# Performance work log

Hardware: AMD Instinct MI355X
Metric: run time of the kernel (lower is better)

## Reference

```python
import jax, jax.numpy as jnp
import numpy as np
import math

N = 50000
E = 1600000
A = 100          # num_atoms
H = 64           # hidden_dim / node_dim
L = 5            # num_layers
NB = 8           # num_basis
LMAX = 2
CUTOFF = 5.0


def setup_inputs() -> dict:
    key = jax.random.key(0)
    ks = jax.random.split(key, 32)
    s = 0.05
    inp = {
        'atomic_numbers': jax.random.randint(ks[0], (N,), 0, A),
        'pos': jax.random.normal(ks[1], (N, 3), jnp.float32) * 2.0,
        'edge_index': jax.random.randint(ks[2], (2, E), 0, N),
        # GaussianBasis widths
        'widths': jnp.ones((NB,), jnp.float32) * 0.5,
        # node embedding
        'embed': jax.random.normal(ks[3], (A, H), jnp.float32),
        # per-layer params, stacked on leading layer dim
        'rad_w1': jax.random.normal(ks[4], (L, NB, H), jnp.float32) * s,
        'rad_b1': jnp.zeros((L, H), jnp.float32),
        'rad_w2': jax.random.normal(ks[5], (L, H, H * (LMAX + 1)), jnp.float32) * s,
        'rad_b2': jnp.zeros((L, H * (LMAX + 1)), jnp.float32),
        'self_w': jax.random.normal(ks[6], (L, H, H), jnp.float32) * s,
        'self_b': jnp.zeros((L, H), jnp.float32),
        'proj_w': jax.random.normal(ks[7], (L, 2 * H, H), jnp.float32) * s,
        'proj_b': jnp.zeros((L, H), jnp.float32),
        'mlp_w1': jax.random.normal(ks[8], (L, H, 2 * H), jnp.float32) * s,
        'mlp_b1': jnp.zeros((L, 2 * H), jnp.float32),
        'mlp_w2': jax.random.normal(ks[9], (L, 2 * H, H), jnp.float32) * s,
        'mlp_b2': jnp.zeros((L, H), jnp.float32),
        'ln_g': jnp.ones((L, H), jnp.float32),
        'ln_b': jnp.zeros((L, H), jnp.float32),
        # readout MLP
        'ro_w1': jax.random.normal(ks[10], (H, H), jnp.float32) * s,
        'ro_b1': jnp.zeros((H,), jnp.float32),
        'ro_w2': jax.random.normal(ks[11], (H, H // 2), jnp.float32) * s,
        'ro_b2': jnp.zeros((H // 2,), jnp.float32),
        'ro_w3': jax.random.normal(ks[12], (H // 2, 1), jnp.float32) * s,
        'ro_b3': jnp.zeros((1,), jnp.float32),
        # per-species reference energies
        'atomic_e': jax.random.normal(ks[13], (A, 1), jnp.float32) * s,
    }
    return inp


def _layer_norm(x, g, b, eps=1e-5):
    mu = jnp.mean(x, axis=-1, keepdims=True)
    var = jnp.var(x, axis=-1, keepdims=True)
    return (x - mu) * jax.lax.rsqrt(var + eps) * g + b


def _spherical_harmonics(edge_vec):
    # real SH up to lmax=2, [E, 9] (computed for fidelity; unused by conv math)
    r = jnp.clip(jnp.linalg.norm(edge_vec, axis=-1), 1e-8, None)
    x, y, z = edge_vec[:, 0] / r, edge_vec[:, 1] / r, edge_vec[:, 2] / r
    x2, y2, z2 = x * x, y * y, z * z
    return jnp.stack([
        jnp.full_like(x, 0.28209479177387814),
        -0.4886025119029199 * y, 0.4886025119029199 * z, -0.4886025119029199 * x,
        1.0925484305920792 * x * y, -1.0925484305920792 * y * z,
        0.94617469575756 * z2 - 0.31539156525252 * (x2 + y2),
        -1.0925484305920792 * x * z, 0.5462742152960396 * (x2 - y2),
    ], axis=-1)


def _forward(atomic_numbers, pos, edge_index, widths, embed,
             rad_w1, rad_b1, rad_w2, rad_b2, self_w, self_b, proj_w, proj_b,
             mlp_w1, mlp_b1, mlp_w2, mlp_b2, ln_g, ln_b,
             ro_w1, ro_b1, ro_w2, ro_b2, ro_w3, ro_b3, atomic_e):
    n = pos.shape[0]
    row, col = edge_index[0], edge_index[1]
    edge_vec = pos[col] - pos[row]                          # [E,3]
    edge_len = jnp.linalg.norm(edge_vec, axis=-1, keepdims=True)  # [E,1]

    # GaussianBasis
    xr = edge_len / CUTOFF
    cut = 0.5 * (jnp.cos(xr * math.pi) + 1.0)
    cut = cut * (edge_len < CUTOFF).astype(jnp.float32)     # [E,1]
    centers = jnp.linspace(0.0, CUTOFF, NB)
    diff = edge_len - centers                               # [E,NB]
    edge_rbf = jnp.exp(-0.5 * (diff / jnp.clip(widths, 0.1, None)) ** 2) * cut

    edge_sh = _spherical_harmonics(edge_vec)  # computed but unused, as in source

    feats = embed[atomic_numbers]                           # [N,H]
    for i in range(L):
        # radial net -> per-edge weights [E, H*(lmax+1)]
        w = jax.nn.silu(edge_rbf @ rad_w1[i] + rad_b1[i]) @ rad_w2[i] + rad_b2[i]
        # messages: node_j[:,:,None] * w.view(E,H,lmax+1) summed over last dim
        # == node_j * w.reshape(E,H,lmax+1).sum(-1)
        wsum = w.reshape(-1, H, LMAX + 1).sum(axis=-1)      # [E,H]
        messages = feats[col] * wsum                        # gather + multiply
        agg = jax.ops.segment_sum(messages, row, num_segments=n)  # scatter-add
        self_out = feats @ self_w[i] + self_b[i]
        conv_out = jnp.concatenate([self_out, agg], axis=-1) @ proj_w[i] + proj_b[i]
        upd = jax.nn.silu(conv_out @ mlp_w1[i] + mlp_b1[i]) @ mlp_w2[i] + mlp_b2[i]
        feats = _layer_norm(feats + upd, ln_g[i], ln_b[i])

    h = jax.nn.silu(feats @ ro_w1 + ro_b1)
    h = jax.nn.silu(h @ ro_w2 + ro_b2)
    atomic_energies = h @ ro_w3 + ro_b3                     # [N,1]
    atomic_energies = atomic_energies + atomic_e[atomic_numbers]
    return atomic_energies.sum()                            # batch=None path


def reference(atomic_numbers, pos, edge_index, widths, embed,
              rad_w1, rad_b1, rad_w2, rad_b2, self_w, self_b, proj_w, proj_b,
              mlp_w1, mlp_b1, mlp_w2, mlp_b2, ln_g, ln_b,
              ro_w1, ro_b1, ro_w2, ro_b2, ro_w3, ro_b3, atomic_e):
    return _forward(atomic_numbers, pos, edge_index, widths, embed,
                    rad_w1, rad_b1, rad_w2, rad_b2, self_w, self_b, proj_w, proj_b,
                    mlp_w1, mlp_b1, mlp_w2, mlp_b2, ln_g, ln_b,
                    ro_w1, ro_b1, ro_w2, ro_b2, ro_w3, ro_b3, atomic_e)
```

## Files before the change

kernel.cpp:

```cpp
#include <hip/hip_runtime.h>
#include <math.h>

constexpr int N_NODES = 50000;
constexpr int N_EDGES = 1600000;
constexpr int HDIM    = 64;
constexpr int NLAYER  = 5;
constexpr int NBASIS  = 8;
constexpr int TLUT    = 512;
constexpr float CUT_R = 5.0f;
constexpr float PI_F  = 3.14159265358979f;

constexpr int NBKT = 196;
constexpr int BCAP = 9216;
constexpr int TILE = 1024;

typedef __attribute__((ext_vector_type(8))) short short8;
typedef __attribute__((ext_vector_type(4))) float f32x4;
#define MFMA16 __builtin_amdgcn_mfma_f32_16x16x32_bf16

__device__ __forceinline__ float waveRedSum(float v) {
    for (int off = 32; off > 0; off >>= 1) v += __shfl_xor(v, off, 64);
    return v;
}
__device__ __forceinline__ float siluf(float x) { return x / (1.0f + __expf(-x)); }

__device__ __forceinline__ unsigned int f2bf(float x) {
    unsigned int b = __float_as_uint(x);
    return (b + 0x7fffu + ((b >> 16) & 1u)) >> 16;
}
__device__ __forceinline__ float bf_lo(unsigned int u) { return __uint_as_float(u << 16); }
__device__ __forceinline__ float bf_hi(unsigned int u) { return __uint_as_float(u & 0xffff0000u); }


__global__ void k_embed(const int* __restrict__ an, const float* __restrict__ embed,
                        float* __restrict__ feats, unsigned short* __restrict__ featsbf) {
    int i = blockIdx.x * blockDim.x + threadIdx.x;
    if (i >= N_NODES * HDIM) return;
    int node = i >> 6, h = i & 63;
    float v = embed[an[node] * HDIM + h];
    feats[i] = v;
    featsbf[i] = (unsigned short)f2bf(v);
}

__global__ __launch_bounds__(256) void k_binA(const int* __restrict__ row,
                                              const int* __restrict__ col,
                                              const float* __restrict__ pos,
                                              int* __restrict__ btail,
                                              uint2* __restrict__ binned) {
    __shared__ uint2 ent[TILE];
    __shared__ short bb[TILE];
    __shared__ uint2 sorted[TILE];
    __shared__ int cnt[256], cnt2[256], base[256], gbase[256], scn[256];
    const int tid = threadIdx.x;
    const int t0  = blockIdx.x * TILE;
    const int nv  = min(TILE, N_EDGES - t0);

    cnt[tid] = 0;
    __syncthreads();

    #pragma unroll
    for (int i = 0; i < TILE / 256; ++i) {
        int idx = i * 256 + tid;
        if (idx < nv) {
            int e = t0 + idx;
            int r = row[e], c = col[e];
            float dx = pos[c * 3 + 0] - pos[r * 3 + 0];
            float dy = pos[c * 3 + 1] - pos[r * 3 + 1];
            float dz = pos[c * 3 + 2] - pos[r * 3 + 2];
            float len = sqrtf(dx * dx + dy * dy + dz * dz);
            float t = len * ((float)(TLUT - 1) / CUT_R);
            t = fminf(t, (float)(TLUT - 1));
            unsigned int nn = (unsigned int)(t + 0.5f);
            if (nn > TLUT - 1) nn = TLUT - 1;
            uint2 p;
            p.x = ((unsigned int)c << 16) | nn;
            p.y = (unsigned int)r;
            ent[idx] = p;
            int b = r >> 8;
            bb[idx] = (short)b;
            atomicAdd(&cnt[b], 1);
        }
    }
    __syncthreads();
    int cv = cnt[tid];
    scn[tid] = cv;
    __syncthreads();
    for (int off = 1; off < 256; off <<= 1) {
        int add = (tid >= off) ? scn[tid - off] : 0;
        __syncthreads();
        scn[tid] += add;
        __syncthreads();
    }
    base[tid] = scn[tid] - cv;
    if (tid < NBKT && cv > 0) gbase[tid] = atomicAdd(&btail[tid], cv);
    cnt2[tid] = base[tid];
    __syncthreads();
    #pragma unroll
    for (int i = 0; i < TILE / 256; ++i) {
        int idx = i * 256 + tid;
        if (idx < nv) {
            int b = bb[idx];
            int p = atomicAdd(&cnt2[b], 1);
            sorted[p] = ent[idx];
        }
    }
    __syncthreads();
    for (int s = tid; s < nv; s += 256) {
        uint2 p = sorted[s];
        int b = (int)(p.y >> 8);
        binned[(size_t)b * BCAP + gbase[b] + (s - base[b])] = p;
    }
}

__global__ void k_scanB(const int* __restrict__ btail, int* __restrict__ bbase) {
    __shared__ int s[256];
    int t = threadIdx.x;
    int v = (t < NBKT) ? btail[t] : 0;
    s[t] = v; __syncthreads();
    for (int off = 1; off < 256; off <<= 1) {
        int add = (t >= off) ? s[t - off] : 0;
        __syncthreads();
        s[t] += add;
        __syncthreads();
    }
    if (t < NBKT) bbase[t] = s[t] - v;
}

__global__ __launch_bounds__(256) void k_binB(const uint2* __restrict__ binned,
                                              const int* __restrict__ btail,
                                              const int* __restrict__ bbase,
                                              int* __restrict__ starts,
                                              unsigned int* __restrict__ erec) {
    __shared__ int hist[256];
    __shared__ int scn[256];
    __shared__ int cur[256];
    const int b = blockIdx.x;
    const int node0 = b << 8;
    const int t = threadIdx.x;
    hist[t] = 0;
    __syncthreads();
    const int cnt = btail[b];
    const uint2* src = binned + (size_t)b * BCAP;
    for (int s = t; s < cnt; s += 256)
        atomicAdd(&hist[src[s].y & 255], 1);
    __syncthreads();
    int h = hist[t];
    scn[t] = h;
    __syncthreads();
    for (int off = 1; off < 256; off <<= 1) {
        int add = (t >= off) ? scn[t - off] : 0;
        __syncthreads();
        scn[t] += add;
        __syncthreads();
    }
    int excl = bbase[b] + scn[t] - h;
    int n = node0 + t;
    if (n < N_NODES) starts[n] = excl;
    if (b == 0 && t == 0) starts[N_NODES] = N_EDGES;
    cur[t] = excl;
    __syncthreads();
    for (int s = t; s < cnt; s += 256) {
        uint2 p = src[s];
        int pp = atomicAdd(&cur[p.y & 255], 1);
        erec[pp] = p.x;
    }
}

__global__ void k_prep(const float* __restrict__ rad_w2, const float* __restrict__ self_w,
                       const float* __restrict__ proj_w,
                       float* __restrict__ W2s, float* __restrict__ Wsp) {
    int i = blockIdx.x * blockDim.x + threadIdx.x;
    if (i >= NLAYER * HDIM * HDIM) return;
    int l = i / (HDIM * HDIM); int rem = i % (HDIM * HDIM);
    int k = rem / HDIM; int h = rem % HDIM;
    const float* w = rad_w2 + ((size_t)l * HDIM + k) * (HDIM * 3) + h * 3;
    W2s[i] = w[0] + w[1] + w[2];
    const float* sw = self_w + ((size_t)l * HDIM + k) * HDIM;
    const float* pw = proj_w + (size_t)l * 2 * HDIM * HDIM;
    float acc = 0.f;
    for (int m = 0; m < HDIM; ++m) acc += sw[m] * pw[m * HDIM + h];
    Wsp[i] = acc;
}

__global__ void k_wtr(const float* __restrict__ Wsp, const float* __restrict__ proj_w,
                      const float* __restrict__ mlp_w1, const float* __restrict__ mlp_w2,
                      unsigned short* __restrict__ WspT, unsigned short* __restrict__ PbT,
                      unsigned short* __restrict__ W1T, unsigned short* __restrict__ W2T) {
    int i = blockIdx.x * blockDim.x + threadIdx.x;
    if (i >= NLAYER * 24576) return;
    int l = i / 24576, off = i % 24576;
    if (off < 4096) {
        int n = off >> 6, k = off & 63;
        WspT[(size_t)l * 4096 + off] = (unsigned short)f2bf(Wsp[(size_t)l * 4096 + k * 64 + n]);
    } else if (off < 8192) {
        int o = off - 4096; int n = o >> 6, k = o & 63;
        PbT[(size_t)l * 4096 + o] =
            (unsigned short)f2bf(proj_w[(size_t)l * 8192 + (64 + k) * 64 + n]);
    } else if (off < 16384) {
        int o = off - 8192; int n = o >> 6, k = o & 63;
        W1T[(size_t)l * 8192 + o] = (unsigned short)f2bf(mlp_w1[(size_t)l * 8192 + k * 128 + n]);
    } else {
        int o = off - 16384; int n = o >> 7, k = o & 127;
        W2T[(size_t)l * 8192 + o] = (unsigned short)f2bf(mlp_w2[(size_t)l * 8192 + k * 64 + n]);
    }
}

__global__ void k_rotr(const float* __restrict__ ro_w1, const float* __restrict__ ro_w2,
                       unsigned short* __restrict__ Ro1T, unsigned short* __restrict__ Ro2T) {
    int i = blockIdx.x * blockDim.x + threadIdx.x;
    if (i >= 6144) return;
    if (i < 4096) {
        int n = i >> 6, k = i & 63;
        Ro1T[i] = (unsigned short)f2bf(ro_w1[k * 64 + n]);
    } else {
        int o = i - 4096; int n = o >> 6, k = o & 63;
        Ro2T[o] = (unsigned short)f2bf(ro_w2[k * 32 + n]);
    }
}

__global__ void k_bias(const float* __restrict__ rad_b2, const float* __restrict__ self_b,
                       const float* __restrict__ proj_w, const float* __restrict__ proj_b,
                       float* __restrict__ b2s, float* __restrict__ bsp) {
    int i = blockIdx.x * blockDim.x + threadIdx.x;
    if (i >= NLAYER * HDIM) return;
    int l = i / HDIM, h = i % HDIM;
    const float* rb2 = rad_b2 + l * HDIM * 3 + h * 3;
    b2s[i] = rb2[0] + rb2[1] + rb2[2];
    float acc = proj_b[l * HDIM + h];
    const float* pw = proj_w + (size_t)l * 2 * HDIM * HDIM;
    const float* sb = self_b + l * HDIM;
    for (int m = 0; m < HDIM; ++m) acc += sb[m] * pw[m * HDIM + h];
    bsp[i] = acc;
}

__global__ void k_lut(const float* __restrict__ widths, const float* __restrict__ rad_w1,
                      const float* __restrict__ rad_b1, const float* __restrict__ W2s,
                      const float* __restrict__ b2s, float* __restrict__ lut) {
    int bid = blockIdx.x;
    int l = bid / TLUT, t = bid % TLUT;
    int h = threadIdx.x;
    __shared__ float h1s[HDIM];
    float len = (float)t * (CUT_R / (float)(TLUT - 1));
    float cut = 0.0f;
    if (len < CUT_R) cut = 0.5f * (cosf(len * (PI_F / CUT_R)) + 1.0f);
    float acc = rad_b1[l * HDIM + h];
    for (int b = 0; b < NBASIS; ++b) {
        float wb = fmaxf(widths[b], 0.1f);
        float center = (float)b * (CUT_R / (float)(NBASIS - 1));
        float d = (len - center) / wb;
        float rbf = __expf(-0.5f * d * d) * cut;
        acc += rbf * rad_w1[(l * NBASIS + b) * HDIM + h];
    }
    h1s[h] = siluf(acc);
    __syncthreads();
    float o = b2s[l * HDIM + h];
    const float* w2 = W2s + (size_t)l * HDIM * HDIM;
    for (int k = 0; k < HDIM; ++k) o += h1s[k] * w2[k * HDIM + h];
    lut[(size_t)bid * HDIM + h] = o;
}

__global__ void k_lutb(const float* __restrict__ lut, unsigned short* __restrict__ lutB) {
    int i = blockIdx.x * blockDim.x + threadIdx.x;
    if (i >= NLAYER * TLUT * HDIM) return;
    lutB[i] = (unsigned short)f2bf(lut[i]);
}


__global__ __launch_bounds__(256) void k_agg(const uint4* __restrict__ featsbf4,
                                             const uint4* __restrict__ lutB4_l,
                                             const int* __restrict__ starts,
                                             const unsigned int* __restrict__ erec,
                                             uint4* __restrict__ aggbf4) {
    int wid  = (blockIdx.x * blockDim.x + threadIdx.x) >> 6;
    int lane = threadIdx.x & 63;
    int slot = lane >> 3;
    int j    = lane & 7;
    if (wid >= N_NODES) return;
    int e0 = starts[wid], e1 = starts[wid + 1];
    float a0 = 0, a1 = 0, a2 = 0, a3 = 0, a4 = 0, a5 = 0, a6 = 0, a7 = 0;
    #pragma unroll 2
    for (int e = e0 + slot; e < e1; e += 8) {
        unsigned int rec = erec[e];
        int c  = rec >> 16;
        int i0 = rec & 0xffff;
        uint4 qw = lutB4_l[i0 * 8 + j];
        uint4 fb = featsbf4[(size_t)c * 8 + j];
        a0 += bf_lo(fb.x) * bf_lo(qw.x);
        a1 += bf_hi(fb.x) * bf_hi(qw.x);
        a2 += bf_lo(fb.y) * bf_lo(qw.y);
        a3 += bf_hi(fb.y) * bf_hi(qw.y);
        a4 += bf_lo(fb.z) * bf_lo(qw.z);
        a5 += bf_hi(fb.z) * bf_hi(qw.z);
        a6 += bf_lo(fb.w) * bf_lo(qw.w);
        a7 += bf_hi(fb.w) * bf_hi(qw.w);
    }
    #pragma unroll
    for (int off = 8; off < 64; off <<= 1) {
        a0 += __shfl_xor(a0, off, 64);  a1 += __shfl_xor(a1, off, 64);
        a2 += __shfl_xor(a2, off, 64);  a3 += __shfl_xor(a3, off, 64);
        a4 += __shfl_xor(a4, off, 64);  a5 += __shfl_xor(a5, off, 64);
        a6 += __shfl_xor(a6, off, 64);  a7 += __shfl_xor(a7, off, 64);
    }
    if (slot == 0) {
        uint4 o;
        o.x = f2bf(a0) | (f2bf(a1) << 16);
        o.y = f2bf(a2) | (f2bf(a3) << 16);
        o.z = f2bf(a4) | (f2bf(a5) << 16);
        o.w = f2bf(a6) | (f2bf(a7) << 16);
        aggbf4[(size_t)wid * 8 + j] = o;
    }
}

constexpr int BP = 72;
__global__ __launch_bounds__(256) void k_node(float* __restrict__ feats,
        unsigned short* __restrict__ featsbf,
        const unsigned short* __restrict__ aggbf,
        const unsigned short* __restrict__ WspT_l, const unsigned short* __restrict__ PbT_l,
        const unsigned short* __restrict__ W1T_l, const unsigned short* __restrict__ W2T_l,
        const float* __restrict__ bsp_l,
        const float* __restrict__ mlp_b1_l, const float* __restrict__ mlp_b2_l,
        const float* __restrict__ ln_g_l, const float* __restrict__ ln_b_l) {
    __shared__ unsigned short P[64 * BP];
    __shared__ unsigned short Q[64 * BP];
    __shared__ unsigned short S[64 * BP];
    const int tid  = threadIdx.x;
    const int lane = tid & 63;
    const int wib  = tid >> 6;
    const int mt   = __builtin_amdgcn_readfirstlane(wib);
    const int nb0  = blockIdx.x * 64;
    const int colL = lane & 15;
    const int kgrp = lane >> 4;

    #pragma unroll 4
    for (int i = 0; i < 16; ++i) {
        int r  = wib + i * 4;
        int nd = nb0 + r; nd = (nd < N_NODES) ? nd : (N_NODES - 1);
        P[r * BP + lane] = featsbf[(size_t)nd * 64 + lane];
        Q[r * BP + lane] = aggbf[(size_t)nd * 64 + lane];
    }
    __syncthreads();

    f32x4 acc[4];
    #pragma unroll
    for (int nt = 0; nt < 4; ++nt) {
        float b = bsp_l[nt * 16 + colL];
        acc[nt][0] = b; acc[nt][1] = b; acc[nt][2] = b; acc[nt][3] = b;
    }
    #pragma unroll
    for (int kb = 0; kb < 2; ++kb) {
        short8 ax = *(const short8*)&P[(mt * 16 + colL) * BP + kb * 32 + kgrp * 8];
        short8 aa = *(const short8*)&Q[(mt * 16 + colL) * BP + kb * 32 + kgrp * 8];
        #pragma unroll
        for (int nt = 0; nt < 4; ++nt) {
            short8 bw = *(const short8*)&WspT_l[(nt * 16 + colL) * 64 + kb * 32 + kgrp * 8];
            acc[nt] = MFMA16(ax, bw, acc[nt], 0, 0, 0);
            short8 bp = *(const short8*)&PbT_l[(nt * 16 + colL) * 64 + kb * 32 + kgrp * 8];
            acc[nt] = MFMA16(aa, bp, acc[nt], 0, 0, 0);
        }
    }
    __syncthreads();
    #pragma unroll
    for (int nt = 0; nt < 4; ++nt)
        #pragma unroll
        for (int j = 0; j < 4; ++j)
            P[(mt * 16 + kgrp * 4 + j) * BP + nt * 16 + colL] = (unsigned short)f2bf(acc[nt][j]);
    __syncthreads();

    {
        f32x4 m[8];
        #pragma unroll
        for (int nt = 0; nt < 8; ++nt) {
            float b = mlp_b1_l[nt * 16 + colL];
            m[nt][0] = b; m[nt][1] = b; m[nt][2] = b; m[nt][3] = b;
        }
        #pragma unroll
        for (int kb = 0; kb < 2; ++kb) {
            short8 ac = *(const short8*)&P[(mt * 16 + colL) * BP + kb * 32 + kgrp * 8];
            #pragma unroll
            for (int nt = 0; nt < 8; ++nt) {
                short8 bw = *(const short8*)&W1T_l[(nt * 16 + colL) * 64 + kb * 32 + kgrp * 8];
                m[nt] = MFMA16(ac, bw, m[nt], 0, 0, 0);
            }
        }
        __syncthreads();
        #pragma unroll
        for (int nt = 0; nt < 4; ++nt)
            #pragma unroll
            for (int j = 0; j < 4; ++j)
                Q[(mt * 16 + kgrp * 4 + j) * BP + nt * 16 + colL] =
                    (unsigned short)f2bf(siluf(m[nt][j]));
        #pragma unroll
        for (int nt = 4; nt < 8; ++nt)
            #pragma unroll
            for (int j = 0; j < 4; ++j)
                S[(mt * 16 + kgrp * 4 + j) * BP + (nt - 4) * 16 + colL] =
                    (unsigned short)f2bf(siluf(m[nt][j]));
    }
    __syncthreads();

    f32x4 u[4];
    #pragma unroll
    for (int nt = 0; nt < 4; ++nt) {
        float b = mlp_b2_l[nt * 16 + colL];
        u[nt][0] = b; u[nt][1] = b; u[nt][2] = b; u[nt][3] = b;
    }
    #pragma unroll
    for (int kb = 0; kb < 4; ++kb) {
        short8 am = (kb < 2)
            ? *(const short8*)&Q[(mt * 16 + colL) * BP + kb * 32 + kgrp * 8]
            : *(const short8*)&S[(mt * 16 + colL) * BP + (kb - 2) * 32 + kgrp * 8];
        #pragma unroll
        for (int nt = 0; nt < 4; ++nt) {
            short8 bw = *(const short8*)&W2T_l[(nt * 16 + colL) * 128 + kb * 32 + kgrp * 8];
            u[nt] = MFMA16(am, bw, u[nt], 0, 0, 0);
        }
    }

    float y[4][4];
    float s1[4] = {0, 0, 0, 0}, s2[4] = {0, 0, 0, 0};
    #pragma unroll
    for (int j = 0; j < 4; ++j) {
        int node = nb0 + mt * 16 + kgrp * 4 + j;
        int nds  = (node < N_NODES) ? node : (N_NODES - 1);
        #pragma unroll
        for (int nt = 0; nt < 4; ++nt) {
            float v = feats[(size_t)nds * 64 + nt * 16 + colL] + u[nt][j];
            y[nt][j] = v;
            s1[j] += v; s2[j] += v * v;
        }
    }
    #pragma unroll
    for (int off = 1; off < 16; off <<= 1) {
        #pragma unroll
        for (int j = 0; j < 4; ++j) {
            s1[j] += __shfl_xor(s1[j], off, 64);
            s2[j] += __shfl_xor(s2[j], off, 64);
        }
    }
    float gv[4], bv[4];
    #pragma unroll
    for (int nt = 0; nt < 4; ++nt) {
        gv[nt] = ln_g_l[nt * 16 + colL];
        bv[nt] = ln_b_l[nt * 16 + colL];
    }
    #pragma unroll
    for (int j = 0; j < 4; ++j) {
        int node = nb0 + mt * 16 + kgrp * 4 + j;
        if (node >= N_NODES) continue;
        float mu  = s1[j] * (1.0f / 64.0f);
        float var = s2[j] * (1.0f / 64.0f) - mu * mu;
        float rr  = rsqrtf(var + 1e-5f);
        #pragma unroll
        for (int nt = 0; nt < 4; ++nt) {
            float o = (y[nt][j] - mu) * rr * gv[nt] + bv[nt];
            feats[(size_t)node * 64 + nt * 16 + colL]   = o;
            featsbf[(size_t)node * 64 + nt * 16 + colL] = (unsigned short)f2bf(o);
        }
    }
}


__global__ __launch_bounds__(256) void k_readout(const unsigned short* __restrict__ featsbf,
        const int* __restrict__ an,
        const unsigned short* __restrict__ Ro1T, const unsigned short* __restrict__ Ro2T,
        const float* __restrict__ ro_b1, const float* __restrict__ ro_b2,
        const float* __restrict__ ro_w3, const float* __restrict__ ro_b3,
        const float* __restrict__ atomic_e, float* __restrict__ blockpart) {
    __shared__ unsigned short P[64 * BP];
    __shared__ unsigned short Q[64 * BP];
    __shared__ float sred[256];
    const int tid  = threadIdx.x;
    const int lane = tid & 63;
    const int wib  = tid >> 6;
    const int mt   = __builtin_amdgcn_readfirstlane(wib);
    const int nb0  = blockIdx.x * 64;
    const int colL = lane & 15;
    const int kgrp = lane >> 4;

    #pragma unroll 4
    for (int i = 0; i < 16; ++i) {
        int r  = wib + i * 4;
        int nd = nb0 + r; nd = (nd < N_NODES) ? nd : (N_NODES - 1);
        P[r * BP + lane] = featsbf[(size_t)nd * 64 + lane];
    }
    __syncthreads();

    {
        f32x4 m[4];
        #pragma unroll
        for (int nt = 0; nt < 4; ++nt) {
            float b = ro_b1[nt * 16 + colL];
            m[nt][0] = b; m[nt][1] = b; m[nt][2] = b; m[nt][3] = b;
        }
        #pragma unroll
        for (int kb = 0; kb < 2; ++kb) {
            short8 ax = *(const short8*)&P[(mt * 16 + colL) * BP + kb * 32 + kgrp * 8];
            #pragma unroll
            for (int nt = 0; nt < 4; ++nt) {
                short8 bw = *(const short8*)&Ro1T[(nt * 16 + colL) * 64 + kb * 32 + kgrp * 8];
                m[nt] = MFMA16(ax, bw, m[nt], 0, 0, 0);
            }
        }
        __syncthreads();
        #pragma unroll
        for (int nt = 0; nt < 4; ++nt)
            #pragma unroll
            for (int j = 0; j < 4; ++j)
                Q[(mt * 16 + kgrp * 4 + j) * BP + nt * 16 + colL] =
                    (unsigned short)f2bf(siluf(m[nt][j]));
    }
    __syncthreads();

    f32x4 u[2];
    #pragma unroll
    for (int nt = 0; nt < 2; ++nt) {
        float b = ro_b2[nt * 16 + colL];
        u[nt][0] = b; u[nt][1] = b; u[nt][2] = b; u[nt][3] = b;
    }
    #pragma unroll
    for (int kb = 0; kb < 2; ++kb) {
        short8 am = *(const short8*)&Q[(mt * 16 + colL) * BP + kb * 32 + kgrp * 8];
        #pragma unroll
        for (int nt = 0; nt < 2; ++nt) {
            short8 bw = *(const short8*)&Ro2T[(nt * 16 + colL) * 64 + kb * 32 + kgrp * 8];
            u[nt] = MFMA16(am, bw, u[nt], 0, 0, 0);
        }
    }
    float w3[2];
    #pragma unroll
    for (int nt = 0; nt < 2; ++nt) w3[nt] = ro_w3[nt * 16 + colL];
    float part = 0.0f;
    #pragma unroll
    for (int j = 0; j < 4; ++j) {
        float c = siluf(u[0][j]) * w3[0] + siluf(u[1][j]) * w3[1];
        #pragma unroll
        for (int off = 1; off < 16; off <<= 1) c += __shfl_xor(c, off, 64);
        int node = nb0 + mt * 16 + kgrp * 4 + j;
        if (colL == 0 && node < N_NODES)
            part += c + ro_b3[0] + atomic_e[an[node]];
    }
    sred[tid] = part;
    __syncthreads();
    for (int off = 128; off > 0; off >>= 1) {
        if (tid < off) sred[tid] += sred[tid + off];
        __syncthreads();
    }
    if (tid == 0) blockpart[blockIdx.x] = sred[0];
}

__global__ void k_final(const float* __restrict__ blockpart, int nb, float* __restrict__ out) {
    __shared__ float s[256];
    float acc = 0.f;
    for (int i = threadIdx.x; i < nb; i += 256) acc += blockpart[i];
    s[threadIdx.x] = acc; __syncthreads();
    for (int off = 128; off > 0; off >>= 1) {
        if (threadIdx.x < off) s[threadIdx.x] += s[threadIdx.x + off];
        __syncthreads();
    }
    if (threadIdx.x == 0) out[0] = s[0];
}


extern "C" void kernel_launch(void* const* d_in, const int* in_sizes, int n_in,
                              void* d_out, int out_size, void* d_ws, size_t ws_size,
                              hipStream_t stream) {
    const int*   an       = (const int*)  d_in[0];
    const float* pos      = (const float*)d_in[1];
    const int*   edge     = (const int*)  d_in[2];
    const float* widths   = (const float*)d_in[3];
    const float* embed    = (const float*)d_in[4];
    const float* rad_w1   = (const float*)d_in[5];
    const float* rad_b1   = (const float*)d_in[6];
    const float* rad_w2   = (const float*)d_in[7];
    const float* rad_b2   = (const float*)d_in[8];
    const float* self_w   = (const float*)d_in[9];
    const float* self_b   = (const float*)d_in[10];
    const float* proj_w   = (const float*)d_in[11];
    const float* proj_b   = (const float*)d_in[12];
    const float* mlp_w1   = (const float*)d_in[13];
    const float* mlp_b1   = (const float*)d_in[14];
    const float* mlp_w2   = (const float*)d_in[15];
    const float* mlp_b2   = (const float*)d_in[16];
    const float* ln_g     = (const float*)d_in[17];
    const float* ln_b     = (const float*)d_in[18];
    const float* ro_w1    = (const float*)d_in[19];
    const float* ro_b1    = (const float*)d_in[20];
    const float* ro_w2    = (const float*)d_in[21];
    const float* ro_b2    = (const float*)d_in[22];
    const float* ro_w3    = (const float*)d_in[23];
    const float* ro_b3    = (const float*)d_in[24];
    const float* atomic_e = (const float*)d_in[25];

    char* w = (char*)d_ws;
    auto alloc = [&](size_t bytes) { char* p = w; w += (bytes + 255) & ~(size_t)255; return p; };
    float* feats     = (float*)alloc(sizeof(float) * N_NODES * HDIM);
    unsigned short* featsbf = (unsigned short*)alloc(sizeof(unsigned short) * N_NODES * HDIM);
    unsigned short* aggbf   = (unsigned short*)alloc(sizeof(unsigned short) * N_NODES * HDIM);
    float* lut       = (float*)alloc(sizeof(float) * NLAYER * TLUT * HDIM);
    unsigned short* lutB = (unsigned short*)alloc(sizeof(unsigned short) * NLAYER * TLUT * HDIM);
    float* W2s       = (float*)alloc(sizeof(float) * NLAYER * HDIM * HDIM);
    float* b2s       = (float*)alloc(sizeof(float) * NLAYER * HDIM);
    float* Wsp       = (float*)alloc(sizeof(float) * NLAYER * HDIM * HDIM);
    float* bsp       = (float*)alloc(sizeof(float) * NLAYER * HDIM);
    unsigned short* WspT = (unsigned short*)alloc(sizeof(unsigned short) * NLAYER * 4096);
    unsigned short* PbT  = (unsigned short*)alloc(sizeof(unsigned short) * NLAYER * 4096);
    unsigned short* W1T  = (unsigned short*)alloc(sizeof(unsigned short) * NLAYER * 8192);
    unsigned short* W2T  = (unsigned short*)alloc(sizeof(unsigned short) * NLAYER * 8192);
    unsigned short* Ro1T = (unsigned short*)alloc(sizeof(unsigned short) * 4096);
    unsigned short* Ro2T = (unsigned short*)alloc(sizeof(unsigned short) * 2048);
    unsigned int* erec = (unsigned int*)alloc(sizeof(unsigned int) * N_EDGES);
    uint2* binned    = (uint2*)alloc(sizeof(uint2) * (size_t)NBKT * BCAP);
    int*   btail     = (int*)  alloc(sizeof(int) * 256);
    int*   bbase     = (int*)  alloc(sizeof(int) * 256);
    int*   starts    = (int*)  alloc(sizeof(int) * (N_NODES + 1));
    float* blockpart = (float*)alloc(sizeof(float) * 1024);
    (void)ws_size; (void)in_sizes; (void)n_in; (void)out_size;

    const int* erow = edge;
    const int* ecol = edge + N_EDGES;

    hipMemsetAsync(btail, 0, sizeof(int) * 256, stream);
    k_embed<<<12500, 256, 0, stream>>>(an, embed, feats, featsbf);
    k_binA<<<(N_EDGES + TILE - 1) / TILE, 256, 0, stream>>>(erow, ecol, pos, btail, binned);
    k_scanB<<<1, 256, 0, stream>>>(btail, bbase);
    k_binB<<<NBKT, 256, 0, stream>>>(binned, btail, bbase, starts, erec);
    k_prep<<<80, 256, 0, stream>>>(rad_w2, self_w, proj_w, W2s, Wsp);
    k_wtr<<<(NLAYER * 24576 + 255) / 256, 256, 0, stream>>>(Wsp, proj_w, mlp_w1, mlp_w2,
                                                            WspT, PbT, W1T, W2T);
    k_rotr<<<24, 256, 0, stream>>>(ro_w1, ro_w2, Ro1T, Ro2T);
    k_bias<<<5, 64, 0, stream>>>(rad_b2, self_b, proj_w, proj_b, b2s, bsp);
    k_lut<<<NLAYER * TLUT, 64, 0, stream>>>(widths, rad_w1, rad_b1, W2s, b2s, lut);
    k_lutb<<<(NLAYER * TLUT * HDIM + 255) / 256, 256, 0, stream>>>(lut, lutB);

    for (int l = 0; l < NLAYER; ++l) {
        k_agg<<<12500, 256, 0, stream>>>((const uint4*)featsbf,
                                         (const uint4*)(lutB + (size_t)l * TLUT * HDIM),
                                         starts, erec, (uint4*)aggbf);
        k_node<<<782, 256, 0, stream>>>(feats, featsbf, aggbf,
            WspT + (size_t)l * 4096, PbT + (size_t)l * 4096,
            W1T + (size_t)l * 8192, W2T + (size_t)l * 8192,
            bsp + l * HDIM, mlp_b1 + l * 2 * HDIM, mlp_b2 + l * HDIM,
            ln_g + l * HDIM, ln_b + l * HDIM);
    }

    k_readout<<<782, 256, 0, stream>>>(featsbf, an, Ro1T, Ro2T, ro_b1, ro_b2,
                                       ro_w3, ro_b3, atomic_e, blockpart);
    k_final<<<1, 256, 0, stream>>>(blockpart, 782, (float*)d_out);
}
```

Baseline: 413.6 us.

## Pack binned edge records into 32 bits and widen per-lane aggregation loads

Halves the radial lookup table to 256 entries so the LUT index fits in 8 bits. The edge record can then hold column, LUT index and the low row byte in one 32-bit word, halving the binned intermediate traffic. The binning tile grows to 2048 edges. The aggregation kernel now uses 16 edge slots with 4 lanes each loading two uint4 chunks, trading more registers and a longer shuffle reduction for more edges in flight. The coarser LUT lowers radial-filter resolution, which risks accuracy. It also relies on the node count staying under 65536 for the 16-bit column field.

```diff
diff --git a/kernel.cpp b/kernel.cpp
--- a/kernel.cpp
+++ b/kernel.cpp
@@ -6,22 +6,18 @@
 constexpr int HDIM    = 64;
 constexpr int NLAYER  = 5;
 constexpr int NBASIS  = 8;
-constexpr int TLUT    = 512;
+constexpr int TLUT    = 256;
 constexpr float CUT_R = 5.0f;
 constexpr float PI_F  = 3.14159265358979f;
 
 constexpr int NBKT = 196;
 constexpr int BCAP = 9216;
-constexpr int TILE = 1024;
+constexpr int TILE = 2048;
 
 typedef __attribute__((ext_vector_type(8))) short short8;
 typedef __attribute__((ext_vector_type(4))) float f32x4;
 #define MFMA16 __builtin_amdgcn_mfma_f32_16x16x32_bf16
 
-__device__ __forceinline__ float waveRedSum(float v) {
-    for (int off = 32; off > 0; off >>= 1) v += __shfl_xor(v, off, 64);
-    return v;
-}
 __device__ __forceinline__ float siluf(float x) { return x / (1.0f + __expf(-x)); }
 
 __device__ __forceinline__ unsigned int f2bf(float x) {
@@ -46,10 +42,11 @@
                                               const int* __restrict__ col,
                                               const float* __restrict__ pos,
                                               int* __restrict__ btail,
-                                              uint2* __restrict__ binned) {
-    __shared__ uint2 ent[TILE];
+                                              unsigned int* __restrict__ binned) {
+    __shared__ unsigned int ent[TILE];
     __shared__ short bb[TILE];
-    __shared__ uint2 sorted[TILE];
+    __shared__ unsigned int sorted[TILE];
+    __shared__ short sortedB[TILE];
     __shared__ int cnt[256], cnt2[256], base[256], gbase[256], scn[256];
     const int tid = threadIdx.x;
     const int t0  = blockIdx.x * TILE;
@@ -72,10 +69,7 @@
             t = fminf(t, (float)(TLUT - 1));
             unsigned int nn = (unsigned int)(t + 0.5f);
             if (nn > TLUT - 1) nn = TLUT - 1;
-            uint2 p;
-            p.x = ((unsigned int)c << 16) | nn;
-            p.y = (unsigned int)r;
-            ent[idx] = p;
+            ent[idx] = ((unsigned int)c << 16) | (nn << 8) | ((unsigned int)r & 255u);
             int b = r >> 8;
             bb[idx] = (short)b;
             atomicAdd(&cnt[b], 1);
@@ -101,14 +95,14 @@
         if (idx < nv) {
             int b = bb[idx];
             int p = atomicAdd(&cnt2[b], 1);
-            sorted[p] = ent[idx];
+            sorted[p]  = ent[idx];
+            sortedB[p] = (short)b;
         }
     }
     __syncthreads();
     for (int s = tid; s < nv; s += 256) {
-        uint2 p = sorted[s];
-        int b = (int)(p.y >> 8);
-        binned[(size_t)b * BCAP + gbase[b] + (s - base[b])] = p;
+        int b = sortedB[s];
+        binned[(size_t)b * BCAP + gbase[b] + (s - base[b])] = sorted[s];
     }
 }
 
@@ -126,7 +120,7 @@
     if (t < NBKT) bbase[t] = s[t] - v;
 }
 
-__global__ __launch_bounds__(256) void k_binB(const uint2* __restrict__ binned,
+__global__ __launch_bounds__(256) void k_binB(const unsigned int* __restrict__ binned,
                                               const int* __restrict__ btail,
                                               const int* __restrict__ bbase,
                                               int* __restrict__ starts,
@@ -140,9 +134,9 @@
     hist[t] = 0;
     __syncthreads();
     const int cnt = btail[b];
-    const uint2* src = binned + (size_t)b * BCAP;
+    const unsigned int* src = binned + (size_t)b * BCAP;
     for (int s = t; s < cnt; s += 256)
-        atomicAdd(&hist[src[s].y & 255], 1);
+        atomicAdd(&hist[src[s] & 255u], 1);
     __syncthreads();
     int h = hist[t];
     scn[t] = h;
@@ -160,9 +154,9 @@
     cur[t] = excl;
     __syncthreads();
     for (int s = t; s < cnt; s += 256) {
-        uint2 p = src[s];
-        int pp = atomicAdd(&cur[p.y & 255], 1);
-        erec[pp] = p.x;
+        unsigned int p = src[s];
+        int pp = atomicAdd(&cur[p & 255u], 1);
+        erec[pp] = p;
     }
 }
 
@@ -273,41 +267,48 @@
                                              uint4* __restrict__ aggbf4) {
     int wid  = (blockIdx.x * blockDim.x + threadIdx.x) >> 6;
     int lane = threadIdx.x & 63;
-    int slot = lane >> 3;
-    int j    = lane & 7;
+    int slot = lane >> 2;
+    int j    = lane & 3;
     if (wid >= N_NODES) return;
     int e0 = starts[wid], e1 = starts[wid + 1];
-    float a0 = 0, a1 = 0, a2 = 0, a3 = 0, a4 = 0, a5 = 0, a6 = 0, a7 = 0;
-    #pragma unroll 2
-    for (int e = e0 + slot; e < e1; e += 8) {
+    float a[16];
+    #pragma unroll
+    for (int q = 0; q < 16; ++q) a[q] = 0.f;
+    #pragma unroll 1
+    for (int e = e0 + slot; e < e1; e += 16) {
         unsigned int rec = erec[e];
         int c  = rec >> 16;
-        int i0 = rec & 0xffff;
-        uint4 qw = lutB4_l[i0 * 8 + j];
-        uint4 fb = featsbf4[(size_t)c * 8 + j];
-        a0 += bf_lo(fb.x) * bf_lo(qw.x);
-        a1 += bf_hi(fb.x) * bf_hi(qw.x);
-        a2 += bf_lo(fb.y) * bf_lo(qw.y);
-        a3 += bf_hi(fb.y) * bf_hi(qw.y);
-        a4 += bf_lo(fb.z) * bf_lo(qw.z);
-        a5 += bf_hi(fb.z) * bf_hi(qw.z);
-        a6 += bf_lo(fb.w) * bf_lo(qw.w);
-        a7 += bf_hi(fb.w) * bf_hi(qw.w);
-    }
-    #pragma unroll
-    for (int off = 8; off < 64; off <<= 1) {
-        a0 += __shfl_xor(a0, off, 64);  a1 += __shfl_xor(a1, off, 64);
-        a2 += __shfl_xor(a2, off, 64);  a3 += __shfl_xor(a3, off, 64);
-        a4 += __shfl_xor(a4, off, 64);  a5 += __shfl_xor(a5, off, 64);
-        a6 += __shfl_xor(a6, off, 64);  a7 += __shfl_xor(a7, off, 64);
+        int i0 = (rec >> 8) & 255;
+        uint4 q0 = lutB4_l[i0 * 8 + 2 * j];
+        uint4 q1 = lutB4_l[i0 * 8 + 2 * j + 1];
+        uint4 f0 = featsbf4[(size_t)c * 8 + 2 * j];
+        uint4 f1 = featsbf4[(size_t)c * 8 + 2 * j + 1];
+        a[0]  += bf_lo(f0.x) * bf_lo(q0.x);  a[1]  += bf_hi(f0.x) * bf_hi(q0.x);
+        a[2]  += bf_lo(f0.y) * bf_lo(q0.y);  a[3]  += bf_hi(f0.y) * bf_hi(q0.y);
+        a[4]  += bf_lo(f0.z) * bf_lo(q0.z);  a[5]  += bf_hi(f0.z) * bf_hi(q0.z);
+        a[6]  += bf_lo(f0.w) * bf_lo(q0.w);  a[7]  += bf_hi(f0.w) * bf_hi(q0.w);
+        a[8]  += bf_lo(f1.x) * bf_lo(q1.x);  a[9]  += bf_hi(f1.x) * bf_hi(q1.x);
+        a[10] += bf_lo(f1.y) * bf_lo(q1.y);  a[11] += bf_hi(f1.y) * bf_hi(q1.y);
+        a[12] += bf_lo(f1.z) * bf_lo(q1.z);  a[13] += bf_hi(f1.z) * bf_hi(q1.z);
+        a[14] += bf_lo(f1.w) * bf_lo(q1.w);  a[15] += bf_hi(f1.w) * bf_hi(q1.w);
+    }
+    #pragma unroll
+    for (int off = 4; off < 64; off <<= 1) {
+        #pragma unroll
+        for (int q = 0; q < 16; ++q) a[q] += __shfl_xor(a[q], off, 64);
     }
     if (slot == 0) {
-        uint4 o;
-        o.x = f2bf(a0) | (f2bf(a1) << 16);
-        o.y = f2bf(a2) | (f2bf(a3) << 16);
-        o.z = f2bf(a4) | (f2bf(a5) << 16);
-        o.w = f2bf(a6) | (f2bf(a7) << 16);
-        aggbf4[(size_t)wid * 8 + j] = o;
+        uint4 o0, o1;
+        o0.x = f2bf(a[0])  | (f2bf(a[1])  << 16);
+        o0.y = f2bf(a[2])  | (f2bf(a[3])  << 16);
+        o0.z = f2bf(a[4])  | (f2bf(a[5])  << 16);
+        o0.w = f2bf(a[6])  | (f2bf(a[7])  << 16);
+        o1.x = f2bf(a[8])  | (f2bf(a[9])  << 16);
+        o1.y = f2bf(a[10]) | (f2bf(a[11]) << 16);
+        o1.z = f2bf(a[12]) | (f2bf(a[13]) << 16);
+        o1.w = f2bf(a[14]) | (f2bf(a[15]) << 16);
+        aggbf4[(size_t)wid * 8 + 2 * j]     = o0;
+        aggbf4[(size_t)wid * 8 + 2 * j + 1] = o1;
     }
 }
 
@@ -609,7 +610,7 @@
     unsigned short* Ro1T = (unsigned short*)alloc(sizeof(unsigned short) * 4096);
     unsigned short* Ro2T = (unsigned short*)alloc(sizeof(unsigned short) * 2048);
     unsigned int* erec = (unsigned int*)alloc(sizeof(unsigned int) * N_EDGES);
-    uint2* binned    = (uint2*)alloc(sizeof(uint2) * (size_t)NBKT * BCAP);
+    unsigned int* binned = (unsigned int*)alloc(sizeof(unsigned int) * (size_t)NBKT * BCAP);
     int*   btail     = (int*)  alloc(sizeof(int) * 256);
     int*   bbase     = (int*)  alloc(sizeof(int) * 256);
     int*   starts    = (int*)  alloc(sizeof(int) * (N_NODES + 1));
```

Result: slower. 447.8 us (+8.3%).
